# Optimization experiments

Measured on AMD Instinct MI355X. Metric: run time of the kernel, lower is better.

## Reference

```python
import jax, jax.numpy as jnp
import numpy as np

EPS = 1e-8

def squash(s, axis=-1):
    sq = jnp.sum(s * s, axis=axis, keepdims=True)
    return (sq / (1.0 + sq)) * s / jnp.sqrt(sq + EPS)

def conv3d(x, w, b, stride=1):
    y = jax.lax.conv_general_dilated(x, w, (stride,) * 3, 'VALID',
                                     dimension_numbers=('NCDHW', 'OIDHW', 'NCDHW'))
    return y + b[None, :, None, None, None]

def deconv3d(x, w, b, stride, pad, out_pad):
    # torch ConvTranspose3d: w is (Cin, Cout, k, k, k)
    k = w.shape[-1]
    wf = jnp.flip(w, axis=(2, 3, 4)).transpose(1, 0, 2, 3, 4)  # (Cout, Cin, k, k, k)
    pads = [(k - 1 - pad, k - 1 - pad + out_pad)] * 3
    y = jax.lax.conv_general_dilated(x, wf, (1, 1, 1), pads,
                                     lhs_dilation=(stride,) * 3,
                                     dimension_numbers=('NCDHW', 'OIDHW', 'NCDHW'))
    return y + b[None, :, None, None, None]

def voxel_ids(pcl, n):
    # per-cloud axis-aligned bounding box voxelization (PyntCloud voxelgrid semantics)
    mn = pcl.min(axis=1, keepdims=True)
    mx = pcl.max(axis=1, keepdims=True)
    idx = jnp.floor((pcl - mn) / (mx - mn + 1e-9) * n).astype(jnp.int32)
    idx = jnp.clip(idx, 0, n - 1)
    return idx[..., 0] * (n * n) + idx[..., 1] * n + idx[..., 2]  # (B, P) flat voxel id

def setup_inputs() -> dict:
    key = jax.random.key(0)
    ks = jax.random.split(key, 16)
    B, P, C, n = 2, 8192, 128, 24
    s = 0.02
    inp = {
        'pcl': jax.random.uniform(ks[0], (B, P, 3), jnp.float32),
        'pcl_feature': jax.random.normal(ks[1], (B, P, C), jnp.float32),
        'n': n,
        'conv1_w': jax.random.normal(ks[2], (256, 128, 5, 5, 5), jnp.float32) * s,
        'conv1_b': jnp.zeros((256,), jnp.float32),
        'conv2_w': jax.random.normal(ks[3], (256, 256, 5, 5, 5), jnp.float32) * s,
        'conv2_b': jnp.zeros((256,), jnp.float32),
        'prim_w': jax.random.normal(ks[4], (256, 256, 9, 9, 9), jnp.float32) * s,
        'prim_b': jnp.zeros((256,), jnp.float32),
        'route_w': jax.random.normal(ks[5], (50, 2048, 64, 8), jnp.float32) * s,
        'dec1_w': jax.random.normal(ks[6], (50, 128, 3, 3, 3), jnp.float32) * s,
        'dec1_b': jnp.zeros((128,), jnp.float32),
        'dec2_w': jax.random.normal(ks[7], (128, 512, 3, 3, 3), jnp.float32) * s,
        'dec2_b': jnp.zeros((512,), jnp.float32),
    }
    return inp

def reference(pcl, pcl_feature, n, conv1_w, conv1_b, conv2_w, conv2_b,
              prim_w, prim_b, route_w, dec1_w, dec1_b, dec2_w, dec2_b):
    B, P, C = pcl_feature.shape
    vid = voxel_ids(pcl, n)  # (B, P)
    # pcl2vox: scatter-add point features into dense voxel grid
    flat_ids = (jnp.arange(B)[:, None] * (n ** 3) + vid).reshape(-1)
    mesh = jax.ops.segment_sum(pcl_feature.reshape(B * P, C), flat_ids,
                               num_segments=B * n ** 3)
    mesh = mesh.reshape(B, n, n, n, C).transpose(0, 4, 1, 2, 3)  # (B, C, n, n, n)
    # conv encoder: 24 -> 20 -> 16
    h = jax.nn.relu(conv3d(mesh, conv1_w, conv1_b))
    h = jax.nn.relu(conv3d(h, conv2_w, conv2_b))  # (B, 256, 16, 16, 16)
    # primary capsules: k=9 s=2 -> (B, 256, 4, 4, 4) -> (B, 2048, 8), squash
    p = conv3d(h, prim_w, prim_b, stride=2)
    u = p.reshape(B, 32, 8, 64).transpose(0, 1, 3, 2).reshape(B, 2048, 8)
    u = squash(u)
    # dynamic routing: u_hat[b,j,i,d] = W[j,i,d,c] u[b,i,c]
    u_hat = jnp.einsum('jidc,bic->bjid', route_w, u)  # (B, 50, 2048, 64)
    b_log = jnp.zeros((B, 50, 2048), u_hat.dtype)
    n_iter = 1
    v = None
    for _ in range(n_iter):
        c = jax.nn.softmax(b_log, axis=1)
        s = jnp.einsum('bji,bjid->bjd', c, u_hat)
        v = squash(s)  # (B, 50, 64)
        b_log = b_log + jnp.einsum('bjid,bjd->bji', u_hat, v)
    # decoder: (B, 50, 4, 4, 4) -> (B, 128, 12^3) -> (B, 512, 24^3)
    r = v.reshape(B, 50, 4, 4, 4)
    d = jax.nn.relu(deconv3d(r, dec1_w, dec1_b, 3, 0, 0))
    d = jax.nn.relu(deconv3d(d, dec2_w, dec2_b, 2, 1, 1))  # (B, 512, 24, 24, 24)
    # vox2pcl: gather per-point features from voxel grid
    d_flat = d.reshape(B, 512, n ** 3)
    out = jnp.take_along_axis(d_flat, vid[:, None, :], axis=2)  # (B, 512, P)
    return out.transpose(0, 2, 1)  # (B, P, 512)
```

## Files before the change

### kernel.cpp

```cpp
#include <hip/hip_runtime.h>
#include <cstdint>
#include <cstddef>

typedef _Float16 h8 __attribute__((ext_vector_type(8)));
typedef _Float16 h4 __attribute__((ext_vector_type(4)));
typedef float    f32x4 __attribute__((ext_vector_type(4)));

#define B_   2
#define P_   8192
#define NVOX 24
#define N3   13824

#define MESHS_OFF 0ull
#define M16_OFF   14155776ull
#define H1CL_OFF  28311552ull
#define WB_OFF    44695552ull
#define WB2C_OFF  44695552ull
#define H2P_OFF   0ull
#define PPART_OFF 25165824ull
#define PR1_OFF   53477376ull
#define WBD_OFF   0ull
#define D2H_OFF   10616832ull
#define D1CL_OFF  38928384ull
#define VID_OFF   63504384ull
#define UBUF_OFF  63700992ull
#define SBUF_OFF  63832064ull
#define VBUF_OFF  63857664ull

#define M16_PL   3538944ull
#define H1_PL    4096000ull
#define D1_PL    442368ull

__device__ inline void split2(float x, _Float16& a0, _Float16& a1)
{
    a0 = (_Float16)x;
    float r = x - (float)a0;
    a1 = (_Float16)(r * 2048.0f);
}

__device__ inline void gload16(const void* g, void* l)
{
    __builtin_amdgcn_global_load_lds(
        (const __attribute__((address_space(1))) char*)g,
        (__attribute__((address_space(3))) char*)l, 16, 0, 0);
}

__device__ inline void tapDecode(int cls, int ti, int& kd, int& kh, int& kw)
{
    int px = (cls >> 2) & 1, py = (cls >> 1) & 1, pz = cls & 1;
    int tiz = pz ? (ti & 1) : 0;
    int t1  = ti >> pz;
    int tiy = py ? (t1 & 1) : 0;
    int tix = t1 >> py;
    kd = px ? tix*2 : 1;
    kh = py ? tiy*2 : 1;
    kw = pz ? tiz*2 : 1;
}

__global__ __launch_bounds__(256)
void k_vid(const float* __restrict__ pcl, int* __restrict__ vid)
{
    int b = blockIdx.x;
    const float* pb = pcl + (size_t)b * P_ * 3;
    float mn[3] = {3e38f, 3e38f, 3e38f};
    float mx[3] = {-3e38f, -3e38f, -3e38f};
    for (int p = threadIdx.x; p < P_; p += 256) {
        #pragma unroll
        for (int d = 0; d < 3; ++d) {
            float v = pb[p*3 + d];
            mn[d] = fminf(mn[d], v);
            mx[d] = fmaxf(mx[d], v);
        }
    }
    __shared__ float red[6][256];
    #pragma unroll
    for (int d = 0; d < 3; ++d) { red[d][threadIdx.x] = mn[d]; red[3+d][threadIdx.x] = mx[d]; }
    __syncthreads();
    for (int s = 128; s > 0; s >>= 1) {
        if (threadIdx.x < (unsigned)s) {
            #pragma unroll
            for (int d = 0; d < 3; ++d) {
                red[d][threadIdx.x]   = fminf(red[d][threadIdx.x],   red[d][threadIdx.x + s]);
                red[3+d][threadIdx.x] = fmaxf(red[3+d][threadIdx.x], red[3+d][threadIdx.x + s]);
            }
        }
        __syncthreads();
    }
    float mn0 = red[0][0], mn1 = red[1][0], mn2 = red[2][0];
    float dd0 = red[3][0] - mn0 + 1e-9f;
    float dd1 = red[4][0] - mn1 + 1e-9f;
    float dd2 = red[5][0] - mn2 + 1e-9f;
    for (int p = threadIdx.x; p < P_; p += 256) {
        float fx = (pb[p*3+0] - mn0) / dd0 * 24.0f;
        float fy = (pb[p*3+1] - mn1) / dd1 * 24.0f;
        float fz = (pb[p*3+2] - mn2) / dd2 * 24.0f;
        int ix = (int)floorf(fx); ix = ix < 0 ? 0 : (ix > 23 ? 23 : ix);
        int iy = (int)floorf(fy); iy = iy < 0 ? 0 : (iy > 23 ? 23 : iy);
        int iz = (int)floorf(fz); iz = iz < 0 ? 0 : (iz > 23 ? 23 : iz);
        vid[b*P_ + p] = ix*576 + iy*24 + iz;
    }
}

__global__ __launch_bounds__(256)
void k_scatter(const float* __restrict__ feat, const int* __restrict__ vid,
               float* __restrict__ meshS)
{
    int g = blockIdx.x*256 + threadIdx.x;
    int c  = g & 127;
    int bp = g >> 7;
    int v  = vid[bp];
    int b  = bp >> 13;
    atomicAdd(&meshS[((size_t)b*N3 + v)*128 + c], feat[g]);
}

__global__ __launch_bounds__(256)
void k_meshsplit(const float* __restrict__ meshS, _Float16* __restrict__ m16)
{
    int g = blockIdx.x*256 + threadIdx.x;
    int e = g*4;
    float4 a = *(const float4*)(meshS + e);
    h4 v0, v1;
    float xs[4] = {a.x, a.y, a.z, a.w};
    #pragma unroll
    for (int j = 0; j < 4; ++j) {
        _Float16 t0, t1; split2(xs[j], t0, t1);
        v0[j] = t0; v1[j] = t1;
    }
    *(h4*)(m16 + e)          = v0;
    *(h4*)(m16 + M16_PL + e) = v1;
}

__global__ __launch_bounds__(256)
void k_splitw1(const float* __restrict__ W, char* __restrict__ Wb)
{
    int g = blockIdx.x*256 + threadIdx.x;
    int el   = g & 8191;
    int tile = g >> 13;
    int m = tile / 250, c = tile - m*250;
    int co = el >> 6, kl = el & 63;
    int kg = c*64 + kl;
    int kid = kg >> 7, ci = kg & 127;
    float x = W[((size_t)((m*128 + co)*128 + ci))*125 + kid];
    _Float16 a0, a1; split2(x, a0, a1);
    char* dst = Wb + (size_t)tile*32768 + (co*128 + ((kl*2) ^ ((co&7)<<4)));
    *(_Float16*)(dst)         = a0;
    *(_Float16*)(dst + 16384) = a1;
}

__global__ __launch_bounds__(256)
void k_splitw2(const float* __restrict__ W, char* __restrict__ Wb, int cBase, int NC)
{
    int g = blockIdx.x*256 + threadIdx.x;
    int el   = g & 8191;
    int tile = g >> 13;
    int m = tile / NC, cl = tile - m*NC;
    int c = cBase + cl;
    int co = el >> 6, kl = el & 63;
    int kg = c*64 + kl;
    int kid = kg >> 8, ci = kg & 255;
    float x = W[((size_t)((m*128 + co)*256 + ci))*125 + kid];
    _Float16 a0, a1; split2(x, a0, a1);
    char* dst = Wb + (size_t)tile*32768 + (co*128 + ((kl*2) ^ ((co&7)<<4)));
    *(_Float16*)(dst)         = a0;
    *(_Float16*)(dst + 16384) = a1;
}

__global__ __launch_bounds__(256)
void k_splitwd2p(const float* __restrict__ W, char* __restrict__ Wb)
{
    int g = blockIdx.x*256 + threadIdx.x;
    int el   = g & 8191;
    int tile = g >> 13;
    int mG = tile / 54, chunkG = tile - mG*54;
    int co = el >> 6, kl = el & 63;
    int rem = chunkG, cls = 0;
    for (int c = 0; c < 8; ++c) {
        int cc = 2 << __popc(c);
        if (rem < cc) { cls = c; break; }
        rem -= cc;
    }
    int k  = rem*64 + kl;
    int ti = k >> 7;
    int ci = k & 127;
    int kd, kh, kw;
    tapDecode(cls, ti, kd, kh, kw);
    int kid = kd*9 + kh*3 + kw;
    float x = W[((size_t)ci*512 + (mG*128 + co))*27 + kid];
    _Float16 a0, a1; split2(x, a0, a1);
    char* dst = Wb + (size_t)tile*32768 + (co*128 + ((kl*2) ^ ((co&7)<<4)));
    *(_Float16*)(dst)         = a0;
    *(_Float16*)(dst + 16384) = a1;
}

__global__ __launch_bounds__(256, 3)
void k_conv1(const _Float16* __restrict__ m16, const char* __restrict__ Wb,
             const float* __restrict__ bias, _Float16* __restrict__ h1cl)
{
    extern __shared__ char lds[];
    const int tid = threadIdx.x;
    const int l   = tid & 63;
    const int w   = tid >> 6;
    const int wm  = w >> 1, wn = w & 1;
    const int n0  = blockIdx.x * 64;
    const int m   = blockIdx.y;

    const _Float16* preP[4];
    #pragma unroll
    for (int i = 0; i < 4; ++i) {
        int g   = w*4096 + i*1024 + l*16;
        int ver = g >> 13;
        int dd  = g & 8191;
        int nl  = dd >> 7;
        int lg  = (dd & 127) ^ ((nl & 7) << 4);
        int klocal = lg >> 1;
        int n  = n0 + nl;
        int b2 = n / 8000;
        int so = n - b2*8000;
        int x = so/400, y = (so/20)%20, z = so%20;
        preP[i] = m16 + (size_t)ver*M16_PL
                      + ((size_t)(b2*13824 + x*576 + y*24 + z))*128 + klocal;
    }

    const int swz = (l & 7) << 4;
    const int qo  = (l >> 4) << 4;
    const int plF = (l & 15)*128 + (qo ^ (swz & 0x30)) + (swz & 0x40);

    f32x4 acc0[4][2], acc1[4][2];
    const f32x4 zz = {0.f, 0.f, 0.f, 0.f};
    #pragma unroll
    for (int a = 0; a < 4; ++a)
        #pragma unroll
        for (int b = 0; b < 2; ++b) { acc0[a][b] = zz; acc1[a][b] = zz; }

    for (int c = 0; c < 250; ++c) {
        int kid = c >> 1;
        int kd = kid/25, rr = kid - kd*25, kh = rr/5, kw = rr - kh*5;
        int koff = (kd*576 + kh*24 + kw)*128 + (c & 1)*64;

        __syncthreads();
        {
            const char* wsrc = (const char*)Wb + ((size_t)(m*250 + c))*32768 + w*8192;
            #pragma unroll
            for (int i = 0; i < 8; ++i)
                gload16(wsrc + i*1024 + l*16, lds + w*8192 + i*1024);
            #pragma unroll
            for (int i = 0; i < 4; ++i)
                gload16(preP[i] + koff, lds + 32768 + w*4096 + i*1024);
        }
        __syncthreads();

        #pragma unroll
        for (int ks = 0; ks < 2; ++ks) {
            const int kx = ks ? 64 : 0;
            h8 af[2][4], bf[2][2];
            #pragma unroll
            for (int v = 0; v < 2; ++v) {
                #pragma unroll
                for (int mf = 0; mf < 4; ++mf)
                    af[v][mf] = *(const h8*)(lds + v*16384 + (wm*64 + mf*16)*128 + (plF ^ kx));
                #pragma unroll
                for (int nf = 0; nf < 2; ++nf)
                    bf[v][nf] = *(const h8*)(lds + 32768 + v*8192 + (wn*32 + nf*16)*128 + (plF ^ kx));
            }
            #pragma unroll
            for (int mf = 0; mf < 4; ++mf)
                #pragma unroll
                for (int nf = 0; nf < 2; ++nf) {
                    acc0[mf][nf] = __builtin_amdgcn_mfma_f32_16x16x32_f16(af[0][mf], bf[0][nf], acc0[mf][nf], 0,0,0);
                    acc1[mf][nf] = __builtin_amdgcn_mfma_f32_16x16x32_f16(af[0][mf], bf[1][nf], acc1[mf][nf], 0,0,0);
                    acc1[mf][nf] = __builtin_amdgcn_mfma_f32_16x16x32_f16(af[1][mf], bf[0][nf], acc1[mf][nf], 0,0,0);
                }
        }
    }

    const float s1 = 4.8828125e-04f;
    #pragma unroll
    for (int mf = 0; mf < 4; ++mf)
        #pragma unroll
        for (int nf = 0; nf < 2; ++nf) {
            f32x4 r = acc0[mf][nf] + s1*acc1[mf][nf];
            int co = m*128 + wm*64 + mf*16 + ((l>>4)<<2);
            int n  = n0 + wn*32 + nf*16 + (l&15);
            size_t base = (size_t)n*256 + co;
            h4 v0, v1;
            #pragma unroll
            for (int rr = 0; rr < 4; ++rr) {
                float x = fmaxf(r[rr] + bias[co + rr], 0.f);
                _Float16 t0, t1; split2(x, t0, t1);
                v0[rr] = t0; v1[rr] = t1;
            }
            *(h4*)(h1cl + base)         = v0;
            *(h4*)(h1cl + H1_PL + base) = v1;
        }
}

__global__ __launch_bounds__(256, 2)
void k_conv2(const _Float16* __restrict__ h1cl, const char* __restrict__ Wb,
             float* __restrict__ h2p, int cBase, int NSt, int accum)
{
    extern __shared__ char lds[];
    const int tid = threadIdx.x;
    const int l   = tid & 63;
    const int w   = tid >> 6;
    const int wm  = w >> 1, wn = w & 1;
    const int n0  = blockIdx.x * 128;
    const int m   = blockIdx.y;
    const int per = (NSt + (int)gridDim.z - 1) / (int)gridDim.z;
    const int cl0 = blockIdx.z * per;
    const int cl1 = min(NSt, cl0 + per);

    const _Float16* preP[8];
    #pragma unroll
    for (int i = 0; i < 8; ++i) {
        int g   = w*8192 + i*1024 + l*16;
        int ver = g >> 14;
        int dd  = g & 16383;
        int nl  = dd >> 7;
        int lg  = (dd & 127) ^ ((nl & 7) << 4);
        int klocal = lg >> 1;
        int n = n0 + nl;
        int b2 = n >> 12, so = n & 4095;
        int x = so >> 8, y = (so >> 4) & 15, z = so & 15;
        preP[i] = h1cl + (size_t)ver*H1_PL
                       + ((size_t)(b2*8000 + x*400 + y*20 + z))*256 + klocal;
    }

    const int swz = (l & 7) << 4;
    const int qo  = (l >> 4) << 4;
    const int plF = (l & 15)*128 + (qo ^ (swz & 0x30)) + (swz & 0x40);

    f32x4 acc0[4][4], acc1[4][4];
    const f32x4 zz = {0.f, 0.f, 0.f, 0.f};
    #pragma unroll
    for (int a = 0; a < 4; ++a)
        #pragma unroll
        for (int b = 0; b < 4; ++b) { acc0[a][b] = zz; acc1[a][b] = zz; }

    for (int cl = cl0; cl < cl1; ++cl) {
        int cg = cBase + cl;
        int kid = cg >> 2;
        int kd = kid/25, rr = kid - kd*25, kh = rr/5, kw = rr - kh*5;
        int koff = (kd*400 + kh*20 + kw)*256 + (cg & 3)*64;

        __syncthreads();
        {
            const char* wsrc = (const char*)Wb + ((size_t)(m*NSt + cl))*32768 + w*8192;
            #pragma unroll
            for (int i = 0; i < 8; ++i)
                gload16(wsrc + i*1024 + l*16, lds + w*8192 + i*1024);
            #pragma unroll
            for (int i = 0; i < 8; ++i)
                gload16(preP[i] + koff, lds + 32768 + w*8192 + i*1024);
        }
        __syncthreads();

        #pragma unroll
        for (int ks = 0; ks < 2; ++ks) {
            const int kx = ks ? 64 : 0;
            h8 af[2][4], bf[2][4];
            #pragma unroll
            for (int v = 0; v < 2; ++v) {
                #pragma unroll
                for (int mf = 0; mf < 4; ++mf)
                    af[v][mf] = *(const h8*)(lds + v*16384 + (wm*64 + mf*16)*128 + (plF ^ kx));
                #pragma unroll
                for (int nf = 0; nf < 4; ++nf)
                    bf[v][nf] = *(const h8*)(lds + 32768 + v*16384 + (wn*64 + nf*16)*128 + (plF ^ kx));
            }
            #pragma unroll
            for (int mf = 0; mf < 4; ++mf)
                #pragma unroll
                for (int nf = 0; nf < 4; ++nf) {
                    acc0[mf][nf] = __builtin_amdgcn_mfma_f32_16x16x32_f16(af[0][mf], bf[0][nf], acc0[mf][nf], 0,0,0);
                    acc1[mf][nf] = __builtin_amdgcn_mfma_f32_16x16x32_f16(af[0][mf], bf[1][nf], acc1[mf][nf], 0,0,0);
                    acc1[mf][nf] = __builtin_amdgcn_mfma_f32_16x16x32_f16(af[1][mf], bf[0][nf], acc1[mf][nf], 0,0,0);
                }
        }
    }

    const float s1 = 4.8828125e-04f;
    float* oz = h2p + (size_t)blockIdx.z * 2097152;
    #pragma unroll
    for (int mf = 0; mf < 4; ++mf)
        #pragma unroll
        for (int nf = 0; nf < 4; ++nf) {
            f32x4 r = acc0[mf][nf] + s1*acc1[mf][nf];
            int co = m*128 + wm*64 + mf*16 + ((l>>4)<<2);
            int n  = n0 + wn*64 + nf*16 + (l&15);
            int b2 = n >> 12, so = n & 4095;
            #pragma unroll
            for (int rr = 0; rr < 4; ++rr) {
                size_t idx = ((size_t)(b2*256 + co + rr))*4096 + so;
                if (accum) oz[idx] += r[rr];
                else       oz[idx]  = r[rr];
            }
        }
}

__global__ __launch_bounds__(256)
void k_h2epi(float* __restrict__ p0, const float* __restrict__ bias)
{
    int g = blockIdx.x*256 + threadIdx.x;
    int e = g*4;
    int co = (e >> 12) & 255;
    float4 a = *(const float4*)(p0 + e);
    float4 b = *(const float4*)(p0 + 2097152 + e);
    float4 c = *(const float4*)(p0 + 4194304 + e);
    float bb = bias[co];
    float4 r;
    r.x = fmaxf(a.x + b.x + c.x + bb, 0.f);
    r.y = fmaxf(a.y + b.y + c.y + bb, 0.f);
    r.z = fmaxf(a.z + b.z + c.z + bb, 0.f);
    r.w = fmaxf(a.w + b.w + c.w + bb, 0.f);
    *(float4*)(p0 + e) = r;
}

template<int CIN, int KD, int STRIDE, int IND, int OUTD>
__global__ __launch_bounds__(256, 2)
void k_gemm_conv(const float* __restrict__ in, const float* __restrict__ W,
                 float* __restrict__ out)
{
    constexpr int KD2  = KD*KD;
    constexpr int K3   = KD*KD*KD;
    constexpr int IND2 = IND*IND;
    constexpr int IND3 = IND2*IND;
    constexpr int OUT2 = OUTD*OUTD;
    constexpr int OUT3 = OUT2*OUTD;
    constexpr int KTOT = CIN*K3;
    constexpr int NCH  = KTOT/16;

    const int tid  = threadIdx.x;
    const int mIdx = tid >> 4;
    const int nIdx = tid & 15;
    const int n0   = blockIdx.x * 128;
    const int co0  = blockIdx.y * 128;
    const int per  = NCH / (int)gridDim.z;
    const int c0   = blockIdx.z * per;
    const int c1   = c0 + per;

    __shared__ float As[16][132];
    __shared__ float Bs[16][132];

    const int nB    = n0 + (tid & 127);
    const int kHalf = tid >> 7;
    int bB = nB / OUT3;
    int sB = nB - bB*OUT3;
    int xB = sB / OUT2;
    int yB = (sB / OUTD) % OUTD;
    int zB = sB % OUTD;
    const float* inB = in + (size_t)bB*CIN*IND3
                          + (xB*STRIDE)*IND2 + (yB*STRIDE)*IND + (zB*STRIDE);
    const int cB  = tid & 127;
    const int qB  = cB >> 2;
    const int bpos = ((((qB & 1) << 4) | (qB >> 1)) << 2) | (cB & 3);

    const int aCo = tid >> 2;
    const int aKq = (tid & 3) * 4;
    const int qA  = aCo >> 2;
    const int apos = ((((qA & 1) << 4) | (qA >> 1)) << 2) | (aCo & 3);
    const float* Wr0 = W + (size_t)(co0 + aCo)*KTOT + aKq;
    const float* Wr1 = W + (size_t)(co0 + 64 + aCo)*KTOT + aKq;

    float acc[8][8];
    #pragma unroll
    for (int i = 0; i < 8; ++i)
        #pragma unroll
        for (int j = 0; j < 8; ++j) acc[i][j] = 0.f;

    for (int c = c0; c < c1; ++c) {
        const int kb = c*16;
        float4 a0 = *(const float4*)(Wr0 + kb);
        float4 a1 = *(const float4*)(Wr1 + kb);
        float bv[8];
        #pragma unroll
        for (int p = 0; p < 8; ++p) {
            int k  = kb + p*2 + kHalf;
            int ci = k / K3;
            int r  = k - ci*K3;
            int kd = r / KD2;
            int r2 = r - kd*KD2;
            int kh = r2 / KD;
            int kw = r2 - kh*KD;
            bv[p] = inB[ci*IND3 + kd*IND2 + kh*IND + kw];
        }
        __syncthreads();
        As[aKq+0][apos] = a0.x; As[aKq+1][apos] = a0.y;
        As[aKq+2][apos] = a0.z; As[aKq+3][apos] = a0.w;
        As[aKq+0][apos+32] = a1.x; As[aKq+1][apos+32] = a1.y;
        As[aKq+2][apos+32] = a1.z; As[aKq+3][apos+32] = a1.w;
        #pragma unroll
        for (int p = 0; p < 8; ++p) Bs[p*2 + kHalf][bpos] = bv[p];
        __syncthreads();
        #pragma unroll
        for (int kk = 0; kk < 16; ++kk) {
            float af[8], bf[8];
            *(float4*)&af[0] = *(const float4*)&As[kk][mIdx*4];
            *(float4*)&af[4] = *(const float4*)&As[kk][64 + mIdx*4];
            *(float4*)&bf[0] = *(const float4*)&Bs[kk][nIdx*4];
            *(float4*)&bf[4] = *(const float4*)&Bs[kk][64 + nIdx*4];
            #pragma unroll
            for (int i = 0; i < 8; ++i)
                #pragma unroll
                for (int j = 0; j < 8; ++j)
                    acc[i][j] += af[i]*bf[j];
        }
    }

    float* oz = out + (size_t)blockIdx.z * (2*256*OUT3);
    #pragma unroll
    for (int j = 0; j < 8; ++j) {
        int n = n0 + nIdx*8 + j;
        int b = n / OUT3;
        int s = n - b*OUT3;
        float* o = oz + ((size_t)b*256 + co0 + mIdx*8)*OUT3 + s;
        #pragma unroll
        for (int i = 0; i < 8; ++i)
            o[(size_t)i*OUT3] = acc[i][j];
    }
}

__global__ __launch_bounds__(256)
void k_pr1(const float* __restrict__ pp, float* __restrict__ out1)
{
    int e = blockIdx.x*256 + threadIdx.x;
    int y = blockIdx.y;
    const float* src = pp + (size_t)y*27*32768 + e;
    float a = 0.f;
    #pragma unroll
    for (int j = 0; j < 27; ++j) a += src[(size_t)j*32768];
    out1[y*32768 + e] = a;
}

__global__ __launch_bounds__(256)
void k_pr2(const float* __restrict__ out1, const float* __restrict__ pbias,
           float* __restrict__ u)
{
    int g = blockIdx.x*256 + threadIdx.x;
    int b = g >> 11;
    int i = g & 2047;
    int cap = i >> 6;
    int s   = i & 63;
    float vals[8];
    float sq = 0.f;
    #pragma unroll
    for (int c = 0; c < 8; ++c) {
        size_t base = ((size_t)(b*256) + cap*8 + c)*64 + s;
        float a = 0.f;
        #pragma unroll
        for (int j = 0; j < 8; ++j) a += out1[(size_t)j*32768 + base];
        float x = a + pbias[cap*8 + c];
        vals[c] = x;
        sq += x*x;
    }
    float scale = (sq / (1.f + sq)) / sqrtf(sq + 1e-8f);
    #pragma unroll
    for (int c = 0; c < 8; ++c) u[(size_t)g*8 + c] = vals[c]*scale;
}

__global__ __launch_bounds__(256)
void k_route(const float* __restrict__ Wr, const float* __restrict__ u,
             float* __restrict__ s_buf)
{
    int j  = blockIdx.x;
    int i0 = blockIdx.y * 256;
    __shared__ float us[2*256*8];
    for (int idx = threadIdx.x; idx < 4096; idx += 256) {
        int b = idx >> 11;
        us[idx] = u[(size_t)b*16384 + (size_t)i0*8 + (idx & 2047)];
    }
    __syncthreads();
    int tid = threadIdx.x;
    int cc  = tid & 7;
    const float* Wj = Wr + (size_t)j*2048*512 + (size_t)i0*512;
    float a00 = 0.f, a01 = 0.f, a10 = 0.f, a11 = 0.f;
    for (int i = 0; i < 256; ++i) {
        float w0 = Wj[(size_t)i*512 + tid];
        float w1 = Wj[(size_t)i*512 + tid + 256];
        float u0 = us[i*8 + cc];
        float u1 = us[2048 + i*8 + cc];
        a00 += w0*u0; a01 += w1*u0; a10 += w0*u1; a11 += w1*u1;
    }
    __syncthreads();
    float* red = us;
    red[tid] = a00; red[256 + tid] = a01; red[512 + tid] = a10; red[768 + tid] = a11;
    __syncthreads();
    if (tid < 128) {
        int b = tid >> 6, d = tid & 63;
        const float* rb = red + b*512 + (d >> 5)*256 + (d & 31)*8;
        float s = 0.f;
        #pragma unroll
        for (int c2 = 0; c2 < 8; ++c2) s += rb[c2];
        atomicAdd(&s_buf[((size_t)b*50 + j)*64 + d], s * (1.0f/50.0f));
    }
}

__global__ __launch_bounds__(64)
void k_squash_v(const float* __restrict__ s_buf, float* __restrict__ v_buf)
{
    int row = blockIdx.x;
    int d   = threadIdx.x;
    float s  = s_buf[row*64 + d];
    float sq = s*s;
    #pragma unroll
    for (int o = 32; o > 0; o >>= 1) sq += __shfl_xor(sq, o);
    float scale = (sq / (1.f + sq)) / sqrtf(sq + 1e-8f);
    v_buf[row*64 + d] = s*scale;
}

__global__ __launch_bounds__(256)
void k_dec1(const float* __restrict__ v, const float* __restrict__ W,
            const float* __restrict__ bias, _Float16* __restrict__ d1cl)
{
    int g  = blockIdx.x*256 + threadIdx.x;
    int co = g & 127;
    int t  = g >> 7;
    int o  = t % 1728;
    int b  = t / 1728;
    int ox = o / 144, oy = (o/12) % 12, oz = o % 12;
    int ix = ox/3, ka = ox - 3*ix;
    int iy = oy/3, kb = oy - 3*iy;
    int iz = oz/3, kc = oz - 3*iz;
    int widx = ka*9 + kb*3 + kc;
    int sidx = ix*16 + iy*4 + iz;
    float s = 0.f;
    for (int ci = 0; ci < 50; ++ci)
        s += v[((size_t)b*50 + ci)*64 + sidx] * W[((size_t)ci*128 + co)*27 + widx];
    float x = fmaxf(s + bias[co], 0.f);
    _Float16 a0, a1; split2(x, a0, a1);
    size_t base = (size_t)(b*1728 + o)*128 + co;
    d1cl[base]         = a0;
    d1cl[base + D1_PL] = a1;
}

__global__ __launch_bounds__(256, 3)
void k_dec2p(const _Float16* __restrict__ d1cl, const char* __restrict__ Wb,
             const float* __restrict__ bias, float* __restrict__ out, int coBase)
{
    extern __shared__ char lds[];
    const int tid = threadIdx.x;
    const int l   = tid & 63;
    const int w   = tid >> 6;
    const int wm  = w >> 1, wn = w & 1;
    const int cls = blockIdx.z;
    const int px  = (cls >> 2) & 1, py = (cls >> 1) & 1, pz = cls & 1;
    const int n0  = blockIdx.x * 64;
    const int m   = blockIdx.y;
    const int mG  = (coBase >> 7) + m;

    int cb = 0;
    for (int c = 0; c < cls; ++c) cb += 2 << __popc(c);
    const int nch = 2 << __popc(cls);

    const int nRow = tid & 63;
    const int q    = tid >> 6;
    const int nT   = n0 + nRow;
    const int b2s  = nT / 1728;
    const int rs   = nT - b2s*1728;
    const int oxh  = rs/144, oyh = (rs/12)%12, ozh = rs%12;
    const int posB = b2s*1728;
    const int bw0 = 32768 + nRow*128 + ((q*32)      ^ ((nRow&7)<<4));
    const int bw1 = 32768 + nRow*128 + ((q*32 + 16) ^ ((nRow&7)<<4));

    const int swz = (l & 7) << 4;
    const int qo  = (l >> 4) << 4;
    const int plF = (l & 15)*128 + (qo ^ (swz & 0x30)) + (swz & 0x40);

    f32x4 acc0[4][2], acc1[4][2];
    const f32x4 zz = {0.f, 0.f, 0.f, 0.f};
    #pragma unroll
    for (int a = 0; a < 4; ++a)
        #pragma unroll
        for (int b = 0; b < 2; ++b) { acc0[a][b] = zz; acc1[a][b] = zz; }

    const h8 z8 = {};
    for (int c = 0; c < nch; ++c) {
        int ti = c >> 1, ch = c & 1;
        int kd, kh, kw;
        tapDecode(cls, ti, kd, kh, kw);
        int txh = oxh + (px && kd == 0);
        int tyh = oyh + (py && kh == 0);
        int tzh = ozh + (pz && kw == 0);
        bool ok = (txh < 12) && (tyh < 12) && (tzh < 12);
        const _Float16* src = d1cl + (size_t)(posB + txh*144 + tyh*12 + tzh)*128
                                   + ch*64 + q*16;
        h8 b0a = *(const h8*)(src);
        h8 b0b = *(const h8*)(src + 8);
        h8 b1a = *(const h8*)(src + D1_PL);
        h8 b1b = *(const h8*)(src + D1_PL + 8);

        __syncthreads();
        {
            const char* wsrc = (const char*)Wb + ((size_t)(mG*54 + cb + c))*32768 + w*8192;
            #pragma unroll
            for (int i = 0; i < 8; ++i)
                gload16(wsrc + i*1024 + l*16, lds + w*8192 + i*1024);
        }
        *(h8*)(lds + bw0)         = ok ? b0a : z8;
        *(h8*)(lds + bw1)         = ok ? b0b : z8;
        *(h8*)(lds + 8192 + bw0)  = ok ? b1a : z8;
        *(h8*)(lds + 8192 + bw1)  = ok ? b1b : z8;
        __syncthreads();

        #pragma unroll
        for (int ks = 0; ks < 2; ++ks) {
            const int kx = ks ? 64 : 0;
            h8 af[2][4], bf[2][2];
            #pragma unroll
            for (int v = 0; v < 2; ++v) {
                #pragma unroll
                for (int mf = 0; mf < 4; ++mf)
                    af[v][mf] = *(const h8*)(lds + v*16384 + (wm*64 + mf*16)*128 + (plF ^ kx));
                #pragma unroll
                for (int nf = 0; nf < 2; ++nf)
                    bf[v][nf] = *(const h8*)(lds + 32768 + v*8192 + (wn*32 + nf*16)*128 + (plF ^ kx));
            }
            #pragma unroll
            for (int mf = 0; mf < 4; ++mf)
                #pragma unroll
                for (int nf = 0; nf < 2; ++nf) {
                    acc0[mf][nf] = __builtin_amdgcn_mfma_f32_16x16x32_f16(af[0][mf], bf[0][nf], acc0[mf][nf], 0,0,0);
                    acc1[mf][nf] = __builtin_amdgcn_mfma_f32_16x16x32_f16(af[0][mf], bf[1][nf], acc1[mf][nf], 0,0,0);
                    acc1[mf][nf] = __builtin_amdgcn_mfma_f32_16x16x32_f16(af[1][mf], bf[0][nf], acc1[mf][nf], 0,0,0);
                }
        }
    }

    const float s1 = 4.8828125e-04f;
    #pragma unroll
    for (int mf = 0; mf < 4; ++mf)
        #pragma unroll
        for (int nf = 0; nf < 2; ++nf) {
            f32x4 r = acc0[mf][nf] + s1*acc1[mf][nf];
            int coL = m*128 + wm*64 + mf*16 + ((l>>4)<<2);
            int coG = coBase + coL;
            int nT2 = n0 + wn*32 + nf*16 + (l&15);
            int b2  = nT2 / 1728;
            int r2  = nT2 - b2*1728;
            int ax  = r2/144, ay = (r2/12)%12, az = r2%12;
            int outIdx = b2*13824 + (2*ax + px)*576 + (2*ay + py)*24 + (2*az + pz);
            float4 v;
            v.x = fmaxf(r[0] + bias[coG + 0], 0.f);
            v.y = fmaxf(r[1] + bias[coG + 1], 0.f);
            v.z = fmaxf(r[2] + bias[coG + 2], 0.f);
            v.w = fmaxf(r[3] + bias[coG + 3], 0.f);
            *(float4*)(out + (size_t)outIdx*256 + coL) = v;
        }
}

__global__ __launch_bounds__(256)
void k_gather(const float* __restrict__ d2h, const int* __restrict__ vid,
              float* __restrict__ out, int colOff)
{
    int g  = blockIdx.x*256 + threadIdx.x;
    int qq = g & 63;
    int bp = g >> 6;
    int v  = vid[bp];
    int b  = bp >> 13;
    float4 val = *(const float4*)&d2h[((size_t)(b*N3 + v))*256 + qq*4];
    *(float4*)&out[(size_t)bp*512 + colOff + qq*4] = val;
}

extern "C" void kernel_launch(void* const* d_in, const int* in_sizes, int n_in,
                              void* d_out, int out_size, void* d_ws, size_t ws_size,
                              hipStream_t stream)
{
    (void)in_sizes; (void)n_in; (void)out_size; (void)ws_size;
    const float* pcl  = (const float*)d_in[0];
    const float* feat = (const float*)d_in[1];
    const float* c1w  = (const float*)d_in[3];
    const float* c1b  = (const float*)d_in[4];
    const float* c2w  = (const float*)d_in[5];
    const float* c2b  = (const float*)d_in[6];
    const float* pw   = (const float*)d_in[7];
    const float* pb   = (const float*)d_in[8];
    const float* rw   = (const float*)d_in[9];
    const float* d1w  = (const float*)d_in[10];
    const float* d1b_ = (const float*)d_in[11];
    const float* d2w  = (const float*)d_in[12];
    const float* d2b  = (const float*)d_in[13];

    char* ws = (char*)d_ws;
    float*     meshS  = (float*)(ws + MESHS_OFF);
    _Float16*  m16    = (_Float16*)(ws + M16_OFF);
    _Float16*  h1cl   = (_Float16*)(ws + H1CL_OFF);
    char*      Wb     = ws + WB_OFF;
    char*      Wb2c   = ws + WB2C_OFF;
    float*     h2p    = (float*)(ws + H2P_OFF);
    float*     p_part = (float*)(ws + PPART_OFF);
    float*     pr1    = (float*)(ws + PR1_OFF);
    char*      Wbd    = ws + WBD_OFF;
    float*     d2h    = (float*)(ws + D2H_OFF);
    _Float16*  d1cl   = (_Float16*)(ws + D1CL_OFF);
    int*       vid    = (int*)(ws + VID_OFF);
    float*     u_buf  = (float*)(ws + UBUF_OFF);
    float*     s_buf  = (float*)(ws + SBUF_OFF);
    float*     v_buf  = (float*)(ws + VBUF_OFF);

    k_vid<<<dim3(B_), dim3(256), 0, stream>>>(pcl, vid);

    hipMemsetAsync(meshS, 0, 14155776, stream);
    k_scatter<<<dim3(8192), dim3(256), 0, stream>>>(feat, vid, meshS);
    k_meshsplit<<<dim3(3456), dim3(256), 0, stream>>>(meshS, m16);

    k_splitw1<<<dim3(16000), dim3(256), 0, stream>>>(c1w, Wb);
    k_conv1<<<dim3(250, 2), dim3(256), 49152, stream>>>(m16, Wb, c1b, h1cl);

    k_splitw2<<<dim3(15872), dim3(256), 0, stream>>>(c2w, Wb2c, 0, 248);
    k_conv2<<<dim3(64, 2, 3), dim3(256), 65536, stream>>>(h1cl, Wb2c, h2p, 0, 248, 0);
    k_splitw2<<<dim3(16128), dim3(256), 0, stream>>>(c2w, Wb2c, 248, 252);
    k_conv2<<<dim3(64, 2, 3), dim3(256), 65536, stream>>>(h1cl, Wb2c, h2p, 248, 252, 1);
    k_h2epi<<<dim3(2048), dim3(256), 0, stream>>>(h2p, c2b);

    k_gemm_conv<256,9,2,16,4><<<dim3(1, 2, 216), dim3(256), 0, stream>>>(h2p, pw, p_part);
    k_pr1<<<dim3(128, 8), dim3(256), 0, stream>>>(p_part, pr1);
    k_pr2<<<dim3(16), dim3(256), 0, stream>>>(pr1, pb, u_buf);

    hipMemsetAsync(s_buf, 0, 25600, stream);
    k_route<<<dim3(50, 8), dim3(256), 0, stream>>>(rw, u_buf, s_buf);
    k_squash_v<<<dim3(100), dim3(64), 0, stream>>>(s_buf, v_buf);

    k_dec1<<<dim3(1728), dim3(256), 0, stream>>>(v_buf, d1w, d1b_, d1cl);

    k_splitwd2p<<<dim3(6912), dim3(256), 0, stream>>>(d2w, Wbd);

    k_dec2p<<<dim3(54, 2, 8), dim3(256), 49152, stream>>>(d1cl, Wbd, d2b, d2h, 0);
    k_gather<<<dim3(4096), dim3(256), 0, stream>>>(d2h, vid, (float*)d_out, 0);
    k_dec2p<<<dim3(54, 2, 8), dim3(256), 49152, stream>>>(d1cl, Wbd, d2b, d2h, 256);
    k_gather<<<dim3(4096), dim3(256), 0, stream>>>(d2h, vid, (float*)d_out, 256);
}
```

Baseline: 1.281 ms.

## Widen conv1 N tile to 128 and split K across two blocks with epilogue

conv1 now computes a 128-wide output-position tile per block (4x4 MFMA fragments per wave), which doubles reuse of each loaded weight tile. To keep the grid large enough, the 250-step reduction is split into two halves along grid z. Each half writes fp32 partial sums to a new scratch buffer, and a separate epilogue kernel adds them, applies bias and ReLU, and splits the result into fp16 hi/lo planes. The change costs an extra kernel launch, fp32 partial write and read traffic, a workspace layout reshuffle, and higher register and LDS use per block (occupancy hint lowered from 3 to 2).

```diff
diff --git a/kernel.cpp b/kernel.cpp
--- a/kernel.cpp
+++ b/kernel.cpp
@@ -11,14 +11,15 @@
 #define NVOX 24
 #define N3   13824
 
-#define MESHS_OFF 0ull
-#define M16_OFF   14155776ull
-#define H1CL_OFF  28311552ull
-#define WB_OFF    44695552ull
-#define WB2C_OFF  44695552ull
-#define H2P_OFF   0ull
-#define PPART_OFF 25165824ull
-#define PR1_OFF   53477376ull
+#define M16_OFF   0ull
+#define WB_OFF    14155776ull
+#define MESHS_OFF 30670848ull
+#define C1S_OFF   30670848ull
+#define H1CL_OFF  0ull
+#define WB2C_OFF  16384000ull
+#define H2P_OFF   32899072ull
+#define PPART_OFF 0ull
+#define PR1_OFF   58064896ull
 #define WBD_OFF   0ull
 #define D2H_OFF   10616832ull
 #define D1CL_OFF  38928384ull
@@ -30,6 +31,7 @@
 #define M16_PL   3538944ull
 #define H1_PL    4096000ull
 #define D1_PL    442368ull
+#define C1S_PL   4096000ull
 
 __device__ inline void split2(float x, _Float16& a0, _Float16& a1)
 {
@@ -192,24 +194,25 @@
     *(_Float16*)(dst + 16384) = a1;
 }
 
-__global__ __launch_bounds__(256, 3)
+__global__ __launch_bounds__(256, 2)
 void k_conv1(const _Float16* __restrict__ m16, const char* __restrict__ Wb,
-             const float* __restrict__ bias, _Float16* __restrict__ h1cl)
+             float* __restrict__ c1s)
 {
     extern __shared__ char lds[];
     const int tid = threadIdx.x;
     const int l   = tid & 63;
     const int w   = tid >> 6;
     const int wm  = w >> 1, wn = w & 1;
-    const int n0  = blockIdx.x * 64;
+    const int n0  = blockIdx.x * 128;
     const int m   = blockIdx.y;
-
-    const _Float16* preP[4];
-    #pragma unroll
-    for (int i = 0; i < 4; ++i) {
-        int g   = w*4096 + i*1024 + l*16;
-        int ver = g >> 13;
-        int dd  = g & 8191;
+    const int cl0 = blockIdx.z * 125;
+
+    const _Float16* preP[8];
+    #pragma unroll
+    for (int i = 0; i < 8; ++i) {
+        int g   = w*8192 + i*1024 + l*16;
+        int ver = g >> 14;
+        int dd  = g & 16383;
         int nl  = dd >> 7;
         int lg  = (dd & 127) ^ ((nl & 7) << 4);
         int klocal = lg >> 1;
@@ -225,14 +228,14 @@
     const int qo  = (l >> 4) << 4;
     const int plF = (l & 15)*128 + (qo ^ (swz & 0x30)) + (swz & 0x40);
 
-    f32x4 acc0[4][2], acc1[4][2];
+    f32x4 acc0[4][4], acc1[4][4];
     const f32x4 zz = {0.f, 0.f, 0.f, 0.f};
     #pragma unroll
     for (int a = 0; a < 4; ++a)
         #pragma unroll
-        for (int b = 0; b < 2; ++b) { acc0[a][b] = zz; acc1[a][b] = zz; }
-
-    for (int c = 0; c < 250; ++c) {
+        for (int b = 0; b < 4; ++b) { acc0[a][b] = zz; acc1[a][b] = zz; }
+
+    for (int c = cl0; c < cl0 + 125; ++c) {
         int kid = c >> 1;
         int kd = kid/25, rr = kid - kd*25, kh = rr/5, kw = rr - kh*5;
         int koff = (kd*576 + kh*24 + kw)*128 + (c & 1)*64;
@@ -244,28 +247,28 @@
             for (int i = 0; i < 8; ++i)
                 gload16(wsrc + i*1024 + l*16, lds + w*8192 + i*1024);
             #pragma unroll
-            for (int i = 0; i < 4; ++i)
-                gload16(preP[i] + koff, lds + 32768 + w*4096 + i*1024);
+            for (int i = 0; i < 8; ++i)
+                gload16(preP[i] + koff, lds + 32768 + w*8192 + i*1024);
         }
         __syncthreads();
 
         #pragma unroll
         for (int ks = 0; ks < 2; ++ks) {
             const int kx = ks ? 64 : 0;
-            h8 af[2][4], bf[2][2];
+            h8 af[2][4], bf[2][4];
             #pragma unroll
             for (int v = 0; v < 2; ++v) {
                 #pragma unroll
                 for (int mf = 0; mf < 4; ++mf)
                     af[v][mf] = *(const h8*)(lds + v*16384 + (wm*64 + mf*16)*128 + (plF ^ kx));
                 #pragma unroll
-                for (int nf = 0; nf < 2; ++nf)
-                    bf[v][nf] = *(const h8*)(lds + 32768 + v*8192 + (wn*32 + nf*16)*128 + (plF ^ kx));
+                for (int nf = 0; nf < 4; ++nf)
+                    bf[v][nf] = *(const h8*)(lds + 32768 + v*16384 + (wn*64 + nf*16)*128 + (plF ^ kx));
             }
             #pragma unroll
             for (int mf = 0; mf < 4; ++mf)
                 #pragma unroll
-                for (int nf = 0; nf < 2; ++nf) {
+                for (int nf = 0; nf < 4; ++nf) {
                     acc0[mf][nf] = __builtin_amdgcn_mfma_f32_16x16x32_f16(af[0][mf], bf[0][nf], acc0[mf][nf], 0,0,0);
                     acc1[mf][nf] = __builtin_amdgcn_mfma_f32_16x16x32_f16(af[0][mf], bf[1][nf], acc1[mf][nf], 0,0,0);
                     acc1[mf][nf] = __builtin_amdgcn_mfma_f32_16x16x32_f16(af[1][mf], bf[0][nf], acc1[mf][nf], 0,0,0);
@@ -274,24 +277,37 @@
     }
 
     const float s1 = 4.8828125e-04f;
+    float* oz = c1s + (size_t)blockIdx.z * C1S_PL;
     #pragma unroll
     for (int mf = 0; mf < 4; ++mf)
         #pragma unroll
-        for (int nf = 0; nf < 2; ++nf) {
+        for (int nf = 0; nf < 4; ++nf) {
             f32x4 r = acc0[mf][nf] + s1*acc1[mf][nf];
             int co = m*128 + wm*64 + mf*16 + ((l>>4)<<2);
-            int n  = n0 + wn*32 + nf*16 + (l&15);
-            size_t base = (size_t)n*256 + co;
-            h4 v0, v1;
-            #pragma unroll
-            for (int rr = 0; rr < 4; ++rr) {
-                float x = fmaxf(r[rr] + bias[co + rr], 0.f);
-                _Float16 t0, t1; split2(x, t0, t1);
-                v0[rr] = t0; v1[rr] = t1;
-            }
-            *(h4*)(h1cl + base)         = v0;
-            *(h4*)(h1cl + H1_PL + base) = v1;
-        }
+            int n  = n0 + wn*64 + nf*16 + (l&15);
+            *(f32x4*)(oz + (size_t)n*256 + co) = r;
+        }
+}
+
+__global__ __launch_bounds__(256)
+void k_c1epi(const float* __restrict__ c1s, const float* __restrict__ bias,
+             _Float16* __restrict__ h1cl)
+{
+    int g = blockIdx.x*256 + threadIdx.x;
+    int e = g*4;
+    int co = e & 255;
+    float4 a = *(const float4*)(c1s + e);
+    float4 b = *(const float4*)(c1s + C1S_PL + e);
+    float xs[4] = {a.x + b.x, a.y + b.y, a.z + b.z, a.w + b.w};
+    h4 v0, v1;
+    #pragma unroll
+    for (int j = 0; j < 4; ++j) {
+        float x = fmaxf(xs[j] + bias[co + j], 0.f);
+        _Float16 t0, t1; split2(x, t0, t1);
+        v0[j] = t0; v1[j] = t1;
+    }
+    *(h4*)(h1cl + e)         = v0;
+    *(h4*)(h1cl + H1_PL + e) = v1;
 }
 
 __global__ __launch_bounds__(256, 2)
@@ -780,10 +796,11 @@
     const float* d2b  = (const float*)d_in[13];
 
     char* ws = (char*)d_ws;
+    _Float16*  m16    = (_Float16*)(ws + M16_OFF);
+    char*      Wb     = ws + WB_OFF;
     float*     meshS  = (float*)(ws + MESHS_OFF);
-    _Float16*  m16    = (_Float16*)(ws + M16_OFF);
+    float*     c1s    = (float*)(ws + C1S_OFF);
     _Float16*  h1cl   = (_Float16*)(ws + H1CL_OFF);
-    char*      Wb     = ws + WB_OFF;
     char*      Wb2c   = ws + WB2C_OFF;
     float*     h2p    = (float*)(ws + H2P_OFF);
     float*     p_part = (float*)(ws + PPART_OFF);
@@ -803,7 +820,8 @@
     k_meshsplit<<<dim3(3456), dim3(256), 0, stream>>>(meshS, m16);
 
     k_splitw1<<<dim3(16000), dim3(256), 0, stream>>>(c1w, Wb);
-    k_conv1<<<dim3(250, 2), dim3(256), 49152, stream>>>(m16, Wb, c1b, h1cl);
+    k_conv1<<<dim3(125, 2, 2), dim3(256), 65536, stream>>>(m16, Wb, c1s);
+    k_c1epi<<<dim3(4000), dim3(256), 0, stream>>>(c1s, c1b, h1cl);
 
     k_splitw2<<<dim3(15872), dim3(256), 0, stream>>>(c2w, Wb2c, 0, 248);
     k_conv2<<<dim3(64, 2, 3), dim3(256), 65536, stream>>>(h1cl, Wb2c, h2p, 0, 248, 0);
```

Result: faster. 1.247 ms (-2.7%).
